# Optimization experiments

Hardware: AMD Instinct MI355X
Metric: run time of the kernel (lower is better)

## Reference

```python
import jax, jax.numpy as jnp
import numpy as np

GRID = 128          # grid_size n
C_MARKERS = 32      # marker embed dim C
M_RHS = 64          # number of right-hand sides m
LENGTH_SCALE = 5.0  # spatial Matern length scale
KERNEL_JITTER = 0.01
MARKER_JITTER = 0.01


def _matern15_eigh(n, length_scale):
    # 1D Matern nu=1.5 kernel on linspace(0,1,n), eigendecomposed (as in __init__)
    x = np.linspace(0.0, 1.0, n)
    d = np.abs(x[:, None] - x[None, :]) / length_scale
    s3d = np.sqrt(3.0) * d
    K = (1.0 + s3d) * np.exp(-s3d)
    lam, V = np.linalg.eigh(K)
    return lam.astype(np.float32), V.astype(np.float32)


def setup_inputs() -> dict:
    key = jax.random.key(0)
    k_v, k_e = jax.random.split(key)
    n, C, m = GRID, C_MARKERS, M_RHS

    lam, V = _matern15_eigh(n, LENGTH_SCALE)

    # Marker covariance K_C = E E^T + marker_jitter * I, eigendecomposed
    E = np.asarray(jax.random.normal(k_e, (C, C), dtype=jnp.float32))
    K_C = E @ E.T + MARKER_JITTER * np.eye(C, dtype=np.float32)
    lam_C, V_C = np.linalg.eigh(K_C)

    # triple_eigs[i,j,k] = lam[i]*lam[j]*lam_C[k] + kernel_jitter  (all > 0)
    triple_eigs = (lam[:, None, None] * lam[None, :, None] * lam_C[None, None, :]
                   + KERNEL_JITTER).astype(np.float32)

    v = jax.random.normal(k_v, (n * n * C, m), dtype=jnp.float32)
    return {
        "v": v,
        "V_C": jnp.asarray(V_C.astype(np.float32)),
        "V": jnp.asarray(V),
        "triple_eigs": jnp.asarray(triple_eigs),
    }


def reference(v, V_C, V, triple_eigs):
    """A^{-1} v via triple-Kronecker eigenbasis: 3 forward rotations,
    eigenvalue divide, 3 reverse rotations. v: [n*n*C, m]."""
    n = V.shape[0]
    C = V_C.shape[0]
    m = v.shape[-1]
    V3 = v.reshape(n, n, C, m)
    tmp = jnp.einsum('ijcm,ck->ijkm', V3, V_C)     # rotate marker axis
    tmp = jnp.einsum('ijkm,jb->ibkm', tmp, V)      # rotate spatial y
    tmp = jnp.einsum('ibkm,ia->abkm', tmp, V)      # rotate spatial x
    tmp = tmp / triple_eigs[..., None]             # divide by eigenvalues
    tmp = jnp.einsum('abkm,jb->ajkm', tmp, V)      # un-rotate spatial y
    tmp = jnp.einsum('ajkm,ia->ijkm', tmp, V)      # un-rotate spatial x
    tmp = jnp.einsum('ijkm,ck->ijcm', tmp, V_C)    # un-rotate marker axis
    return tmp.reshape(n * n * C, m)
```

## Files before the change

kernel.cpp:

```cpp
#include <hip/hip_runtime.h>
#include <hip/hip_bf16.h>
#include <stdint.h>


typedef unsigned short ushort_t;
typedef __attribute__((ext_vector_type(8))) short short8;
typedef __attribute__((ext_vector_type(4))) float f32x4;

__device__ __forceinline__ unsigned short f2bf(float f) {
  union { float f; uint32_t u; } v; v.f = f;
  uint32_t u = v.u;
  return (unsigned short)((u + 0x7fffu + ((u >> 16) & 1u)) >> 16);
}

__global__ __launch_bounds__(256) void prep_kernel(
    const float* __restrict__ te, const float* __restrict__ Vg,
    float* __restrict__ rte, ushort_t* __restrict__ Vhg, ushort_t* __restrict__ Vtg) {
  int b = blockIdx.x, t = threadIdx.x;
  if (b < 64) {
    int ab = b * 256 + t;
    #pragma unroll
    for (int k = 0; k < 32; ++k)
      rte[k * 16384 + ab] = 1.0f / te[ab * 32 + k];
  } else {
    int base = (b - 64) * 4096;
    #pragma unroll
    for (int e = 0; e < 16; ++e) {
      int idx = base + e * 256 + t;
      float f = Vg[idx];
      unsigned short us = f2bf(f);
      Vhg[idx] = us;
      Vtg[(idx & 127) * 128 + (idx >> 7)] = us;
    }
  }
}

__global__ __launch_bounds__(256) void pass1_kernel(
    const float* __restrict__ v, const float* __restrict__ VC, ushort_t* __restrict__ W) {
  __shared__ float Xs[8][32][32];
  __shared__ float VCs[32][32];
  int t  = threadIdx.x;
  int id = blockIdx.x;
  int j  = id & 127;
  int it = (id >> 7) & 3;
  int mt = id >> 9;
  int i0 = it * 32, mm0 = mt * 32;

  #pragma unroll
  for (int e = 0; e < 4; ++e) {
    int idx = e * 256 + t;
    VCs[idx >> 5][idx & 31] = VC[idx];
  }
  __syncthreads();

  int mm = t & 31;
  int kq = t >> 5;

  for (int blk = 0; blk < 4; ++blk) {
    int ib = i0 + blk * 8;
    #pragma unroll
    for (int e = 0; e < 8; ++e) {
      int idx4 = e * 256 + t;
      int ii = idx4 >> 8;
      int c  = (idx4 >> 3) & 31;
      int mq = idx4 & 7;
      float4 src = *(const float4*)(v + ((((size_t)(ib + ii) * 128 + j) * 32 + c) * 64 + mm0 + mq * 4));
      *(float4*)&Xs[ii][c][mq * 4] = src;
    }
    __syncthreads();

    float acc[4][8];
    #pragma unroll
    for (int e = 0; e < 4; ++e)
      #pragma unroll
      for (int ii = 0; ii < 8; ++ii) acc[e][ii] = 0.f;

    for (int c = 0; c < 32; ++c) {
      float xv[8];
      #pragma unroll
      for (int ii = 0; ii < 8; ++ii) xv[ii] = Xs[ii][c][mm];
      #pragma unroll
      for (int e = 0; e < 4; ++e) {
        float w = VCs[c][kq * 4 + e];
        #pragma unroll
        for (int ii = 0; ii < 8; ++ii) acc[e][ii] += w * xv[ii];
      }
    }

    #pragma unroll
    for (int e = 0; e < 4; ++e) {
      int k = kq * 4 + e;
      uint32_t w0 = (uint32_t)f2bf(acc[e][0]) | ((uint32_t)f2bf(acc[e][1]) << 16);
      uint32_t w1 = (uint32_t)f2bf(acc[e][2]) | ((uint32_t)f2bf(acc[e][3]) << 16);
      uint32_t w2 = (uint32_t)f2bf(acc[e][4]) | ((uint32_t)f2bf(acc[e][5]) << 16);
      uint32_t w3 = (uint32_t)f2bf(acc[e][6]) | ((uint32_t)f2bf(acc[e][7]) << 16);
      *(uint4*)(W + (((size_t)(k * 64 + mm0 + mm) * 128 + j) * 128 + ib)) =
          make_uint4(w0, w1, w2, w3);
    }
    __syncthreads();
  }
}

__device__ __forceinline__ void gemm128(const ushort_t (*__restrict__ Am)[136],
                                        const ushort_t (*__restrict__ Bm)[136],
                                        int r0, int c0, int lr, int lk, f32x4 acc[2][4]) {
  #pragma unroll
  for (int fr = 0; fr < 2; ++fr)
    #pragma unroll
    for (int fc = 0; fc < 4; ++fc) acc[fr][fc] = (f32x4){0.f, 0.f, 0.f, 0.f};
  #pragma unroll
  for (int kb = 0; kb < 4; ++kb) {
    short8 a[2], b[4];
    #pragma unroll
    for (int fr = 0; fr < 2; ++fr)
      a[fr] = *(const short8*)&Am[r0 + fr * 16 + lr][kb * 32 + lk];
    #pragma unroll
    for (int fc = 0; fc < 4; ++fc)
      b[fc] = *(const short8*)&Bm[c0 + fc * 16 + lr][kb * 32 + lk];
    #pragma unroll
    for (int fr = 0; fr < 2; ++fr)
      #pragma unroll
      for (int fc = 0; fc < 4; ++fc)
        acc[fr][fc] = __builtin_amdgcn_mfma_f32_16x16x32_bf16(a[fr], b[fc], acc[fr][fc], 0, 0, 0);
  }
}

__global__ __launch_bounds__(512, 4) void pass2_kernel(
    const ushort_t* __restrict__ W, const ushort_t* __restrict__ Vhg,
    const ushort_t* __restrict__ Vtg, const float* __restrict__ rte,
    float* __restrict__ U) {
  __shared__ ushort_t Ab[128][136];
  __shared__ ushort_t Vb[128][136];
  int t = threadIdx.x;
  int blk = blockIdx.x;
  int kk = blk >> 6;

  {
    const uint4* Wp = (const uint4*)W + (size_t)blk * 2048;
    const uint4* Vp = (const uint4*)Vtg;
    #pragma unroll
    for (int e = 0; e < 4; ++e) {
      int idx = e * 512 + t;
      int row = idx >> 4, part = idx & 15;
      *(uint4*)&Ab[row][part * 8] = Wp[idx];
      *(uint4*)&Vb[row][part * 8] = Vp[idx];
    }
  }
  __syncthreads();

  int wave = t >> 6, lane = t & 63;
  int r0 = (wave >> 1) * 32, c0 = (wave & 1) * 64;
  int lr = lane & 15;
  int lk = (lane >> 4) * 8;
  int rowreg = (lane >> 4) * 4;

  f32x4 acc[2][4];

  gemm128(Vb, Ab, r0, c0, lr, lk, acc);
  __syncthreads();
  #pragma unroll
  for (int fr = 0; fr < 2; ++fr)
    #pragma unroll
    for (int fc = 0; fc < 4; ++fc)
      #pragma unroll
      for (int r = 0; r < 4; ++r)
        Ab[r0 + fr * 16 + rowreg + r][c0 + fc * 16 + lr] = f2bf(acc[fr][fc][r]);
  __syncthreads();

  gemm128(Ab, Vb, r0, c0, lr, lk, acc);
  #pragma unroll
  for (int fr = 0; fr < 2; ++fr)
    #pragma unroll
    for (int fc = 0; fc < 4; ++fc)
      #pragma unroll
      for (int r = 0; r < 4; ++r) {
        int a = r0 + fr * 16 + rowreg + r;
        int bcol = c0 + fc * 16 + lr;
        acc[fr][fc][r] *= rte[(size_t)kk * 16384 + a * 128 + bcol];
      }
  __syncthreads();
  #pragma unroll
  for (int fr = 0; fr < 2; ++fr)
    #pragma unroll
    for (int fc = 0; fc < 4; ++fc) {
      int bcol = c0 + fc * 16 + lr;
      int abase = r0 + fr * 16 + rowreg;
      uint32_t lo = (uint32_t)f2bf(acc[fr][fc][0]) | ((uint32_t)f2bf(acc[fr][fc][1]) << 16);
      uint32_t hi = (uint32_t)f2bf(acc[fr][fc][2]) | ((uint32_t)f2bf(acc[fr][fc][3]) << 16);
      *(uint2*)&Ab[bcol][abase] = make_uint2(lo, hi);
    }
  {
    const uint4* Vp = (const uint4*)Vhg;
    #pragma unroll
    for (int e = 0; e < 4; ++e) {
      int idx = e * 512 + t;
      int row = idx >> 4, part = idx & 15;
      *(uint4*)&Vb[row][part * 8] = Vp[idx];
    }
  }
  __syncthreads();

  gemm128(Vb, Ab, r0, c0, lr, lk, acc);
  __syncthreads();
  #pragma unroll
  for (int fr = 0; fr < 2; ++fr)
    #pragma unroll
    for (int fc = 0; fc < 4; ++fc)
      #pragma unroll
      for (int r = 0; r < 4; ++r)
        Ab[r0 + fr * 16 + rowreg + r][c0 + fc * 16 + lr] = f2bf(acc[fr][fc][r]);
  __syncthreads();

  gemm128(Ab, Vb, r0, c0, lr, lk, acc);

  float* Ub = U + (size_t)blk * 16384;
  #pragma unroll
  for (int fr = 0; fr < 2; ++fr)
    #pragma unroll
    for (int fc = 0; fc < 4; ++fc)
      #pragma unroll
      for (int r = 0; r < 4; ++r)
        Ub[(r0 + fr * 16 + rowreg + r) * 128 + (c0 + fc * 16 + lr)] = acc[fr][fc][r];
}

__global__ __launch_bounds__(512, 2) void pass3_kernel(
    const float* __restrict__ U, const float* __restrict__ VC, float* __restrict__ out) {
  __shared__ float Ub[32][32][20];
  __shared__ float VCt[32][32];
  int t  = threadIdx.x;
  int id = blockIdx.x;
  int i  = id & 127;
  int jt = (id >> 7) & 3, mt = id >> 9;
  int j0 = jt * 32, mm0 = mt * 16;

  #pragma unroll
  for (int e = 0; e < 2; ++e) {
    int idx = e * 512 + t;
    VCt[idx & 31][idx >> 5] = VC[idx];
  }
  #pragma unroll
  for (int e = 0; e < 8; ++e) {
    int idx4 = e * 512 + t;
    int fr = idx4 >> 3;
    int part = idx4 & 7;
    int k = fr >> 4, mmi = fr & 15;
    float4 u = *(const float4*)(U + ((((size_t)(k * 64 + mm0 + mmi) * 128) + i) * 128 + j0 + part * 4));
    Ub[k][part * 4 + 0][mmi] = u.x;
    Ub[k][part * 4 + 1][mmi] = u.y;
    Ub[k][part * 4 + 2][mmi] = u.z;
    Ub[k][part * 4 + 3][mmi] = u.w;
  }
  __syncthreads();

  int jj = t & 31, ch = t >> 5;
  float acc[16][2];
  #pragma unroll
  for (int q = 0; q < 16; ++q) { acc[q][0] = 0.f; acc[q][1] = 0.f; }

  for (int k = 0; k < 32; ++k) {
    float vc0 = VCt[k][ch * 2];
    float vc1 = VCt[k][ch * 2 + 1];
    #pragma unroll
    for (int m4 = 0; m4 < 4; ++m4) {
      float4 u = *(const float4*)&Ub[k][jj][m4 * 4];
      const float* up = (const float*)&u;
      #pragma unroll
      for (int e = 0; e < 4; ++e) {
        acc[m4 * 4 + e][0] += vc0 * up[e];
        acc[m4 * 4 + e][1] += vc1 * up[e];
      }
    }
  }

  #pragma unroll
  for (int e2 = 0; e2 < 2; ++e2) {
    int c = ch * 2 + e2;
    #pragma unroll
    for (int m4 = 0; m4 < 4; ++m4) {
      float4 o;
      o.x = acc[m4 * 4 + 0][e2];
      o.y = acc[m4 * 4 + 1][e2];
      o.z = acc[m4 * 4 + 2][e2];
      o.w = acc[m4 * 4 + 3][e2];
      *(float4*)(out + ((((size_t)i * 128 + j0 + jj) * 32 + c) * 64 + mm0 + m4 * 4)) = o;
    }
  }
}

extern "C" void kernel_launch(void* const* d_in, const int* in_sizes, int n_in,
                              void* d_out, int out_size, void* d_ws, size_t ws_size,
                              hipStream_t stream) {
  (void)in_sizes; (void)n_in; (void)out_size; (void)ws_size;
  const float* v  = (const float*)d_in[0];
  const float* VC = (const float*)d_in[1];
  const float* Vg = (const float*)d_in[2];
  const float* te = (const float*)d_in[3];
  float* out = (float*)d_out;

  char* ws = (char*)d_ws;
  ushort_t* W   = (ushort_t*)ws;
  float*    U   = (float*)(ws + 67108864);
  float*    rte = (float*)(ws + 67108864 + 134217728);
  ushort_t* Vhg = (ushort_t*)(ws + 203423744);
  ushort_t* Vtg = (ushort_t*)(ws + 203456512);

  prep_kernel<<<68, 256, 0, stream>>>(te, Vg, rte, Vhg, Vtg);
  pass1_kernel<<<1024, 256, 0, stream>>>(v, VC, W);
  pass2_kernel<<<2048, 512, 0, stream>>>(W, Vhg, Vtg, rte, U);
  pass3_kernel<<<2048, 512, 0, stream>>>(U, VC, out);
}
```

Before: 430.8 us.

## Store intermediate U in bf16 and restructure marker-axis rotation kernels

The intermediate U between the spatial GEMM chain and the marker un-rotation now goes through an LDS staging buffer and is written to global memory as bf16 instead of fp32, halving that traffic. The first and last passes are rewritten to process 32 contiguous (i,j) rows per block with 16 RHS columns. The input is converted to bf16 in LDS and the outputs are transposed through LDS so global writes are coalesced. The prep kernel now vectorizes its reciprocal-eigenvalue writes, and the chain kernel's occupancy hint changes from 4 to 2. Precision of the input and of the intermediate drops to bf16, which risks larger numerical error.

```diff
diff --git a/kernel.cpp b/kernel.cpp
--- a/kernel.cpp
+++ b/kernel.cpp
@@ -1,5 +1,4 @@
 #include <hip/hip_runtime.h>
-#include <hip/hip_bf16.h>
 #include <stdint.h>
 
 
@@ -7,97 +6,115 @@
 typedef __attribute__((ext_vector_type(8))) short short8;
 typedef __attribute__((ext_vector_type(4))) float f32x4;
 
-__device__ __forceinline__ unsigned short f2bf(float f) {
+__device__ __forceinline__ ushort_t f2bf(float f) {
   union { float f; uint32_t u; } v; v.f = f;
   uint32_t u = v.u;
-  return (unsigned short)((u + 0x7fffu + ((u >> 16) & 1u)) >> 16);
+  return (ushort_t)((u + 0x7fffu + ((u >> 16) & 1u)) >> 16);
+}
+__device__ __forceinline__ uint32_t pk2(float a, float b) {
+  return (uint32_t)f2bf(a) | ((uint32_t)f2bf(b) << 16);
+}
+__device__ __forceinline__ float bf2f(ushort_t u) {
+  union { uint32_t x; float f; } v; v.x = (uint32_t)u << 16; return v.f;
 }
 
 __global__ __launch_bounds__(256) void prep_kernel(
     const float* __restrict__ te, const float* __restrict__ Vg,
     float* __restrict__ rte, ushort_t* __restrict__ Vhg, ushort_t* __restrict__ Vtg) {
   int b = blockIdx.x, t = threadIdx.x;
-  if (b < 64) {
-    int ab = b * 256 + t;
-    #pragma unroll
-    for (int k = 0; k < 32; ++k)
-      rte[k * 16384 + ab] = 1.0f / te[ab * 32 + k];
+  if (b < 256) {
+    int id = b * 256 + t;
+    int o0 = id * 8;
+    int k = o0 >> 14, ab0 = o0 & 16383;
+    float r[8];
+    #pragma unroll
+    for (int e = 0; e < 8; ++e) r[e] = 1.0f / te[(ab0 + e) * 32 + k];
+    *(float4*)(rte + o0)     = make_float4(r[0], r[1], r[2], r[3]);
+    *(float4*)(rte + o0 + 4) = make_float4(r[4], r[5], r[6], r[7]);
   } else {
-    int base = (b - 64) * 4096;
+    int base = (b - 256) * 4096 + t;
     #pragma unroll
     for (int e = 0; e < 16; ++e) {
-      int idx = base + e * 256 + t;
-      float f = Vg[idx];
-      unsigned short us = f2bf(f);
+      int idx = base + e * 256;
+      ushort_t us = f2bf(Vg[idx]);
       Vhg[idx] = us;
       Vtg[(idx & 127) * 128 + (idx >> 7)] = us;
     }
   }
 }
 
-__global__ __launch_bounds__(256) void pass1_kernel(
+__global__ __launch_bounds__(256) void k1_rot_t(
     const float* __restrict__ v, const float* __restrict__ VC, ushort_t* __restrict__ W) {
-  __shared__ float Xs[8][32][32];
-  __shared__ float VCs[32][32];
-  int t  = threadIdx.x;
-  int id = blockIdx.x;
-  int j  = id & 127;
-  int it = (id >> 7) & 3;
-  int mt = id >> 9;
-  int i0 = it * 32, mm0 = mt * 32;
+  __shared__ ushort_t Xs[32 * 520];
+  __shared__ ushort_t Wt[512 * 32];
+  __shared__ float VCs[1024];
+  int t = threadIdx.x, bid = blockIdx.x;
+  int jc = bid >> 2, mt = bid & 3;
+  int ji0 = jc * 32, mm0 = mt * 16;
+
+  #pragma unroll
+  for (int e = 0; e < 4; ++e) VCs[e * 256 + t] = VC[e * 256 + t];
 
   #pragma unroll
   for (int e = 0; e < 4; ++e) {
-    int idx = e * 256 + t;
-    VCs[idx >> 5][idx & 31] = VC[idx];
-  }
-  __syncthreads();
-
-  int mm = t & 31;
-  int kq = t >> 5;
-
-  for (int blk = 0; blk < 4; ++blk) {
-    int ib = i0 + blk * 8;
-    #pragma unroll
-    for (int e = 0; e < 8; ++e) {
-      int idx4 = e * 256 + t;
-      int ii = idx4 >> 8;
-      int c  = (idx4 >> 3) & 31;
-      int mq = idx4 & 7;
-      float4 src = *(const float4*)(v + ((((size_t)(ib + ii) * 128 + j) * 32 + c) * 64 + mm0 + mq * 4));
-      *(float4*)&Xs[ii][c][mq * 4] = src;
-    }
-    __syncthreads();
-
-    float acc[4][8];
-    #pragma unroll
-    for (int e = 0; e < 4; ++e)
-      #pragma unroll
-      for (int ii = 0; ii < 8; ++ii) acc[e][ii] = 0.f;
-
-    for (int c = 0; c < 32; ++c) {
-      float xv[8];
-      #pragma unroll
-      for (int ii = 0; ii < 8; ++ii) xv[ii] = Xs[ii][c][mm];
-      #pragma unroll
-      for (int e = 0; e < 4; ++e) {
-        float w = VCs[c][kq * 4 + e];
-        #pragma unroll
-        for (int ii = 0; ii < 8; ++ii) acc[e][ii] += w * xv[ii];
-      }
-    }
-
-    #pragma unroll
-    for (int e = 0; e < 4; ++e) {
-      int k = kq * 4 + e;
-      uint32_t w0 = (uint32_t)f2bf(acc[e][0]) | ((uint32_t)f2bf(acc[e][1]) << 16);
-      uint32_t w1 = (uint32_t)f2bf(acc[e][2]) | ((uint32_t)f2bf(acc[e][3]) << 16);
-      uint32_t w2 = (uint32_t)f2bf(acc[e][4]) | ((uint32_t)f2bf(acc[e][5]) << 16);
-      uint32_t w3 = (uint32_t)f2bf(acc[e][6]) | ((uint32_t)f2bf(acc[e][7]) << 16);
-      *(uint4*)(W + (((size_t)(k * 64 + mm0 + mm) * 128 + j) * 128 + ib)) =
-          make_uint4(w0, w1, w2, w3);
-    }
-    __syncthreads();
+    int q = e * 256 + t;
+    int jj = q >> 5, c = q & 31;
+    const float* src = v + (size_t)(ji0 + jj) * 2048 + c * 64 + mm0;
+    float4 f0 = *(const float4*)(src);
+    float4 f1 = *(const float4*)(src + 4);
+    float4 f2 = *(const float4*)(src + 8);
+    float4 f3 = *(const float4*)(src + 12);
+    uint4 lo = make_uint4(pk2(f0.x, f0.y), pk2(f0.z, f0.w), pk2(f1.x, f1.y), pk2(f1.z, f1.w));
+    uint4 hi = make_uint4(pk2(f2.x, f2.y), pk2(f2.z, f2.w), pk2(f3.x, f3.y), pk2(f3.z, f3.w));
+    ushort_t* dst = &Xs[jj * 520 + c * 16];
+    *(uint4*)dst = lo;
+    *(uint4*)(dst + 8) = hi;
+  }
+  __syncthreads();
+
+  int jj = t & 31, kq = t >> 5;
+  float acc[4][16];
+  #pragma unroll
+  for (int e = 0; e < 4; ++e)
+    #pragma unroll
+    for (int q = 0; q < 16; ++q) acc[e][q] = 0.f;
+
+  for (int c = 0; c < 32; ++c) {
+    const ushort_t* xp = &Xs[jj * 520 + c * 16];
+    short8 x0 = *(const short8*)xp;
+    short8 x1 = *(const short8*)(xp + 8);
+    float vc0 = VCs[c * 32 + kq * 4 + 0];
+    float vc1 = VCs[c * 32 + kq * 4 + 1];
+    float vc2 = VCs[c * 32 + kq * 4 + 2];
+    float vc3 = VCs[c * 32 + kq * 4 + 3];
+    #pragma unroll
+    for (int q = 0; q < 8; ++q) {
+      float xf = bf2f((ushort_t)x0[q]);
+      acc[0][q] += vc0 * xf; acc[1][q] += vc1 * xf;
+      acc[2][q] += vc2 * xf; acc[3][q] += vc3 * xf;
+    }
+    #pragma unroll
+    for (int q = 0; q < 8; ++q) {
+      float xf = bf2f((ushort_t)x1[q]);
+      acc[0][8 + q] += vc0 * xf; acc[1][8 + q] += vc1 * xf;
+      acc[2][8 + q] += vc2 * xf; acc[3][8 + q] += vc3 * xf;
+    }
+  }
+
+  #pragma unroll
+  for (int e = 0; e < 4; ++e)
+    #pragma unroll
+    for (int q = 0; q < 16; ++q)
+      Wt[((kq * 4 + e) * 16 + q) * 32 + jj] = f2bf(acc[e][q]);
+  __syncthreads();
+
+  int part = t & 3, rq = t >> 2;
+  #pragma unroll
+  for (int e = 0; e < 8; ++e) {
+    int row = e * 64 + rq;
+    int k = row >> 4, mmi = row & 15;
+    uint4 d = *(const uint4*)&Wt[row * 32 + part * 8];
+    *(uint4*)(W + (size_t)(k * 64 + mm0 + mmi) * 16384 + ji0 + part * 8) = d;
   }
 }
 
@@ -125,10 +142,10 @@
   }
 }
 
-__global__ __launch_bounds__(512, 4) void pass2_kernel(
+__global__ __launch_bounds__(512, 2) void k3_chain(
     const ushort_t* __restrict__ W, const ushort_t* __restrict__ Vhg,
     const ushort_t* __restrict__ Vtg, const float* __restrict__ rte,
-    float* __restrict__ U) {
+    ushort_t* __restrict__ U) {
   __shared__ ushort_t Ab[128][136];
   __shared__ ushort_t Vb[128][136];
   int t = threadIdx.x;
@@ -212,78 +229,84 @@
   __syncthreads();
 
   gemm128(Ab, Vb, r0, c0, lr, lk, acc);
-
-  float* Ub = U + (size_t)blk * 16384;
+  __syncthreads();
   #pragma unroll
   for (int fr = 0; fr < 2; ++fr)
     #pragma unroll
     for (int fc = 0; fc < 4; ++fc)
       #pragma unroll
       for (int r = 0; r < 4; ++r)
-        Ub[(r0 + fr * 16 + rowreg + r) * 128 + (c0 + fc * 16 + lr)] = acc[fr][fc][r];
-}
-
-__global__ __launch_bounds__(512, 2) void pass3_kernel(
-    const float* __restrict__ U, const float* __restrict__ VC, float* __restrict__ out) {
-  __shared__ float Ub[32][32][20];
-  __shared__ float VCt[32][32];
-  int t  = threadIdx.x;
-  int id = blockIdx.x;
-  int i  = id & 127;
-  int jt = (id >> 7) & 3, mt = id >> 9;
-  int j0 = jt * 32, mm0 = mt * 16;
+        Ab[r0 + fr * 16 + rowreg + r][c0 + fc * 16 + lr] = f2bf(acc[fr][fc][r]);
+  __syncthreads();
+
+  {
+    const size_t ub = (size_t)blk * 16384;
+    #pragma unroll
+    for (int e = 0; e < 4; ++e) {
+      int idx = e * 512 + t;
+      int row = idx >> 4, part = idx & 15;
+      *(uint4*)(U + ub + row * 128 + part * 8) = *(const uint4*)&Ab[row][part * 8];
+    }
+  }
+}
+
+__global__ __launch_bounds__(256) void k5_unrot_t(
+    const ushort_t* __restrict__ U, const float* __restrict__ VC, float* __restrict__ out) {
+  __shared__ ushort_t Us[512 * 40];
+  __shared__ float VCs[1024];
+  int t = threadIdx.x, bid = blockIdx.x;
+  int jc = bid >> 2, mt = bid & 3;
+  int jip0 = jc * 32, mm0 = mt * 16;
+
+  #pragma unroll
+  for (int e = 0; e < 4; ++e) VCs[e * 256 + t] = VC[e * 256 + t];
 
   #pragma unroll
   for (int e = 0; e < 2; ++e) {
-    int idx = e * 512 + t;
-    VCt[idx & 31][idx >> 5] = VC[idx];
-  }
-  #pragma unroll
-  for (int e = 0; e < 8; ++e) {
-    int idx4 = e * 512 + t;
-    int fr = idx4 >> 3;
-    int part = idx4 & 7;
-    int k = fr >> 4, mmi = fr & 15;
-    float4 u = *(const float4*)(U + ((((size_t)(k * 64 + mm0 + mmi) * 128) + i) * 128 + j0 + part * 4));
-    Ub[k][part * 4 + 0][mmi] = u.x;
-    Ub[k][part * 4 + 1][mmi] = u.y;
-    Ub[k][part * 4 + 2][mmi] = u.z;
-    Ub[k][part * 4 + 3][mmi] = u.w;
-  }
-  __syncthreads();
-
-  int jj = t & 31, ch = t >> 5;
-  float acc[16][2];
-  #pragma unroll
-  for (int q = 0; q < 16; ++q) { acc[q][0] = 0.f; acc[q][1] = 0.f; }
+    int row = e * 256 + t;
+    int k = row >> 4, mmi = row & 15;
+    const uint4* src = (const uint4*)(U + (size_t)(k * 64 + mm0 + mmi) * 16384 + jip0);
+    ushort_t* dst = &Us[row * 40];
+    *(uint4*)(dst)      = src[0];
+    *(uint4*)(dst + 8)  = src[1];
+    *(uint4*)(dst + 16) = src[2];
+    *(uint4*)(dst + 24) = src[3];
+  }
+  __syncthreads();
+
+  int jj = t & 31, cq = t >> 5;
+  float acc[4][16];
+  #pragma unroll
+  for (int e = 0; e < 4; ++e)
+    #pragma unroll
+    for (int q = 0; q < 16; ++q) acc[e][q] = 0.f;
 
   for (int k = 0; k < 32; ++k) {
-    float vc0 = VCt[k][ch * 2];
-    float vc1 = VCt[k][ch * 2 + 1];
-    #pragma unroll
-    for (int m4 = 0; m4 < 4; ++m4) {
-      float4 u = *(const float4*)&Ub[k][jj][m4 * 4];
-      const float* up = (const float*)&u;
-      #pragma unroll
-      for (int e = 0; e < 4; ++e) {
-        acc[m4 * 4 + e][0] += vc0 * up[e];
-        acc[m4 * 4 + e][1] += vc1 * up[e];
-      }
-    }
-  }
-
-  #pragma unroll
-  for (int e2 = 0; e2 < 2; ++e2) {
-    int c = ch * 2 + e2;
-    #pragma unroll
-    for (int m4 = 0; m4 < 4; ++m4) {
-      float4 o;
-      o.x = acc[m4 * 4 + 0][e2];
-      o.y = acc[m4 * 4 + 1][e2];
-      o.z = acc[m4 * 4 + 2][e2];
-      o.w = acc[m4 * 4 + 3][e2];
-      *(float4*)(out + ((((size_t)i * 128 + j0 + jj) * 32 + c) * 64 + mm0 + m4 * 4)) = o;
-    }
+    float y[16];
+    #pragma unroll
+    for (int q = 0; q < 16; ++q)
+      y[q] = bf2f(Us[(k * 16 + q) * 40 + jj]);
+    float vc0 = VCs[(cq * 4 + 0) * 32 + k];
+    float vc1 = VCs[(cq * 4 + 1) * 32 + k];
+    float vc2 = VCs[(cq * 4 + 2) * 32 + k];
+    float vc3 = VCs[(cq * 4 + 3) * 32 + k];
+    #pragma unroll
+    for (int q = 0; q < 16; ++q) {
+      acc[0][q] += vc0 * y[q]; acc[1][q] += vc1 * y[q];
+      acc[2][q] += vc2 * y[q]; acc[3][q] += vc3 * y[q];
+    }
+  }
+
+  int i = ((jc & 3) << 5) + jj;
+  int j = jc >> 2;
+  float* ob = out + ((size_t)(i * 128 + j) * 32) * 64 + mm0;
+  #pragma unroll
+  for (int e = 0; e < 4; ++e) {
+    float* oc = ob + (size_t)(cq * 4 + e) * 64;
+    *(float4*)(oc)      = make_float4(acc[e][0],  acc[e][1],  acc[e][2],  acc[e][3]);
+    *(float4*)(oc + 4)  = make_float4(acc[e][4],  acc[e][5],  acc[e][6],  acc[e][7]);
+    *(float4*)(oc + 8)  = make_float4(acc[e][8],  acc[e][9],  acc[e][10], acc[e][11]);
+    *(float4*)(oc + 12) = make_float4(acc[e][12], acc[e][13], acc[e][14], acc[e][15]);
   }
 }
 
@@ -298,14 +321,14 @@
   float* out = (float*)d_out;
 
   char* ws = (char*)d_ws;
-  ushort_t* W   = (ushort_t*)ws;
-  float*    U   = (float*)(ws + 67108864);
-  float*    rte = (float*)(ws + 67108864 + 134217728);
-  ushort_t* Vhg = (ushort_t*)(ws + 203423744);
-  ushort_t* Vtg = (ushort_t*)(ws + 203456512);
-
-  prep_kernel<<<68, 256, 0, stream>>>(te, Vg, rte, Vhg, Vtg);
-  pass1_kernel<<<1024, 256, 0, stream>>>(v, VC, W);
-  pass2_kernel<<<2048, 512, 0, stream>>>(W, Vhg, Vtg, rte, U);
-  pass3_kernel<<<2048, 512, 0, stream>>>(U, VC, out);
-}
+  ushort_t* W   = (ushort_t*)(ws);
+  ushort_t* U   = (ushort_t*)(ws + 67108864);
+  float*    rte = (float*)   (ws + 134217728);
+  ushort_t* Vhg = (ushort_t*)(ws + 136314880);
+  ushort_t* Vtg = (ushort_t*)(ws + 136347648);
+
+  prep_kernel<<<260, 256, 0, stream>>>(te, Vg, rte, Vhg, Vtg);
+  k1_rot_t<<<2048, 256, 0, stream>>>(v, VC, W);
+  k3_chain<<<2048, 512, 0, stream>>>(W, Vhg, Vtg, rte, U);
+  k5_unrot_t<<<2048, 256, 0, stream>>>(U, VC, out);
+}
```

After: 400.4 us. 1.08x faster.
